# Kernel optimization log

Hardware: AMD Instinct MI355X
Metric: run time of the kernel (lower is better)

Reference implementation:

```python
import jax, jax.numpy as jnp
import numpy as np


def soft_threshold24(w):
    """2:4 soft-threshold along the last dim: in each contiguous group of 4,
    zero the two smallest magnitudes and shrink the two largest by the
    second-smallest magnitude (sign(w) * relu(|w| - t))."""
    M, N = w.shape
    g = w.reshape(M, N // 4, 4)
    a = jnp.abs(g)
    thr = jnp.sort(a, axis=-1)[..., 1:2]  # 2nd-smallest magnitude per group
    s = jnp.sign(g) * jnp.maximum(a - thr, 0.0)
    return s.reshape(M, N)


def mm_fp16(a, b):
    """fake_fp8_mm: cast operands to fp16, accumulate in fp32."""
    return jnp.matmul(a.astype(jnp.float16), b.astype(jnp.float16),
                      preferred_element_type=jnp.float32)


def setup_inputs() -> dict:
    key = jax.random.key(0)
    k0, k1, k2, k3 = jax.random.split(key, 4)
    B, S, D, R = 4, 2048, 2048, 512
    return {
        "x": jax.random.normal(k0, (B, S, D), jnp.float32),
        "weight_in": jax.random.normal(k1, (D, R), jnp.float32) * 0.02,
        "weight_out": jax.random.normal(k2, (D, R), jnp.float32) * 0.02,
        "bias": jax.random.normal(k3, (D,), jnp.float32) * 0.01,
        "sparse_scale_in": jnp.array(1.0, jnp.float32),
        "sparse_scale_out": jnp.array(1.0, jnp.float32),
    }


def reference(x, weight_in, weight_out, bias, sparse_scale_in, sparse_scale_out):
    B, S, D = x.shape
    # stage 1: x @ sparse24(weight_in) * scale_in  -> [B,S,R]
    win_s = soft_threshold24(weight_in) * sparse_scale_in          # [D, R]
    h = mm_fp16(x.reshape(-1, D), win_s)                            # [B*S, R] fp32
    # stage 2: h @ sparse24(weight_out.T) * scale_out + bias -> [B,S,D]
    wout_s = soft_threshold24(weight_out.T) * sparse_scale_out      # [R, D]
    out = mm_fp16(h, wout_s) + bias                                 # [B*S, D]
    return out.reshape(B, S, D)
```

## Files before the change

kernel.cpp:

```cpp
#include <hip/hip_runtime.h>

typedef _Float16 f16;
typedef _Float16 f16x8 __attribute__((ext_vector_type(8)));
typedef float f32x4 __attribute__((ext_vector_type(4)));

#define BK 32

__device__ __forceinline__ void g2l16(const f16* g, f16* l) {
    __builtin_amdgcn_global_load_lds(
        (const __attribute__((address_space(1))) void*)g,
        (__attribute__((address_space(3))) void*)l, 16, 0, 0);
}

__device__ __forceinline__ float soft1(float a, float thr, float w, float s) {
    return copysignf(fmaxf(a - thr, 0.0f), w) * s;
}

__device__ __forceinline__ float thr4(float a0, float a1, float a2, float a3) {
    float lo01 = fminf(a0, a1), hi01 = fmaxf(a0, a1);
    float lo23 = fminf(a2, a3), hi23 = fmaxf(a2, a3);
    return fminf(fmaxf(lo01, lo23), fminf(hi01, hi23));
}

__global__ __launch_bounds__(256) void prep_kernel(
    const float* __restrict__ x, f16* __restrict__ xh, int n8,
    const float* __restrict__ Wi, f16* __restrict__ winT, const float* __restrict__ sci,
    const float* __restrict__ Wo, f16* __restrict__ woutT, const float* __restrict__ sco,
    int D, int R, int nCastB, int nSpInB)
{
    int b = blockIdx.x;
    int tid = threadIdx.x;
    if (b < nCastB) {
        int i = b * 256 + tid;
        if (i < n8) {
            float4 a = reinterpret_cast<const float4*>(x)[2 * i];
            float4 c = reinterpret_cast<const float4*>(x)[2 * i + 1];
            f16x8 o = {(f16)a.x, (f16)a.y, (f16)a.z, (f16)a.w,
                       (f16)c.x, (f16)c.y, (f16)c.z, (f16)c.w};
            reinterpret_cast<f16x8*>(xh)[i] = o;
        }
    } else if (b < nCastB + nSpInB) {
        int t = (b - nCastB) * 256 + tid;
        int RG = R >> 2;
        if (t >= RG * D) return;
        int rg = t / D, d = t - rg * D;
        float s = *sci;
        float4 w = *reinterpret_cast<const float4*>(Wi + (size_t)d * R + rg * 4);
        float a0 = fabsf(w.x), a1 = fabsf(w.y), a2 = fabsf(w.z), a3 = fabsf(w.w);
        float thr = thr4(a0, a1, a2, a3);
        size_t base = (size_t)(rg * 4) * D + d;
        winT[base]                 = (f16)soft1(a0, thr, w.x, s);
        winT[base + D]             = (f16)soft1(a1, thr, w.y, s);
        winT[base + 2 * (size_t)D] = (f16)soft1(a2, thr, w.z, s);
        winT[base + 3 * (size_t)D] = (f16)soft1(a3, thr, w.w, s);
    } else {
        int t = (b - nCastB - nSpInB) * 256 + tid;
        if (t >= (D >> 2) * R) return;
        int dg = t / R, r = t - dg * R;
        float s = *sco;
        size_t i0 = (size_t)(dg * 4) * R + r;
        float w0 = Wo[i0], w1 = Wo[i0 + R], w2 = Wo[i0 + 2 * (size_t)R], w3 = Wo[i0 + 3 * (size_t)R];
        float a0 = fabsf(w0), a1 = fabsf(w1), a2 = fabsf(w2), a3 = fabsf(w3);
        float thr = thr4(a0, a1, a2, a3);
        woutT[i0]                 = (f16)soft1(a0, thr, w0, s);
        woutT[i0 + R]             = (f16)soft1(a1, thr, w1, s);
        woutT[i0 + 2 * (size_t)R] = (f16)soft1(a2, thr, w2, s);
        woutT[i0 + 3 * (size_t)R] = (f16)soft1(a3, thr, w3, s);
    }
}

template <int TBM, int TBN, typename OT, bool BIAS>
__global__ __launch_bounds__(256) void gemm_bt(
    const f16* __restrict__ A, const f16* __restrict__ Bt, OT* __restrict__ C,
    const float* __restrict__ bias, int M, int N, int K)
{
    constexpr int MI = TBM / 32;
    constexpr int NF = TBN / 32;
    constexpr int HM = TBM / 2;
    constexpr int HN = TBN / 2;
    __shared__ f16 As[2][TBM * BK];
    __shared__ f16 Bs[2][TBN * BK];

    const int tid  = threadIdx.x;
    const int lane = tid & 63;
    const int w    = tid >> 6;
    const int wm   = w & 1;
    const int wn   = w >> 1;
    const int l16  = lane & 15;
    const int quad = lane >> 4;

    const int nbx = N / TBN;
    const int nb  = gridDim.x;
    int d = blockIdx.x;
    int wgid = ((nb & 7) == 0) ? ((d & 7) * (nb >> 3) + (d >> 3)) : d;
    int by = wgid / nbx;
    int bx = wgid - by * nbx;
    const int bm = by * TBM;
    const int bn = bx * TBN;

    const int srow = lane >> 2;
    const int scol = (lane & 3) * 8;
    const f16* gA = A  + (size_t)(bm + w * (TBM / 4) + srow) * K + scol;
    const f16* gB = Bt + (size_t)(bn + w * (TBN / 4) + srow) * K + scol;

    f32x4 acc[MI][NF] = {};

    auto STAGE = [&](int buf, int k0) {
        f16* lA = &As[buf][(w * (TBM / 4)) * BK];
        f16* lB = &Bs[buf][(w * (TBN / 4)) * BK];
#pragma unroll
        for (int i = 0; i < TBM / 64; ++i)
            g2l16(gA + k0 + i * 16 * (size_t)K, lA + i * 16 * BK);
#pragma unroll
        for (int i = 0; i < TBN / 64; ++i)
            g2l16(gB + k0 + i * 16 * (size_t)K, lB + i * 16 * BK);
        __builtin_amdgcn_sched_barrier(0);
    };

    auto COMPUTE = [&](int buf) {
        f16x8 af[MI], bf[NF];
#pragma unroll
        for (int m = 0; m < MI; ++m)
            af[m] = *reinterpret_cast<const f16x8*>(
                &As[buf][(wm * HM + m * 16 + l16) * BK + quad * 8]);
#pragma unroll
        for (int n = 0; n < NF; ++n)
            bf[n] = *reinterpret_cast<const f16x8*>(
                &Bs[buf][(wn * HN + n * 16 + l16) * BK + quad * 8]);
#pragma unroll
        for (int m = 0; m < MI; ++m)
#pragma unroll
            for (int n = 0; n < NF; ++n)
                acc[m][n] = __builtin_amdgcn_mfma_f32_16x16x32_f16(af[m], bf[n], acc[m][n], 0, 0, 0);
    };

    const int nk = K / BK;
    STAGE(0, 0);
    __syncthreads();
    for (int t = 0; t < nk - 2; t += 2) {
        STAGE(1, (t + 1) * BK);
        COMPUTE(0);
        __syncthreads();
        STAGE(0, (t + 2) * BK);
        COMPUTE(1);
        __syncthreads();
    }
    STAGE(1, (nk - 1) * BK);
    COMPUTE(0);
    __syncthreads();
    COMPUTE(1);

#pragma unroll
    for (int m = 0; m < MI; ++m) {
        int row_base = bm + wm * HM + m * 16 + quad * 4;
#pragma unroll
        for (int n = 0; n < NF; ++n) {
            int col = bn + wn * HN + n * 16 + l16;
            float b = BIAS ? bias[col] : 0.0f;
#pragma unroll
            for (int r = 0; r < 4; ++r) {
                float v = acc[m][n][r];
                size_t idx = (size_t)(row_base + r) * N + col;
                if constexpr (BIAS) C[idx] = (OT)(v + b);
                else                C[idx] = (OT)v;
            }
        }
    }
}

extern "C" void kernel_launch(void* const* d_in, const int* in_sizes, int n_in,
                              void* d_out, int out_size, void* d_ws, size_t ws_size,
                              hipStream_t stream)
{
    const float* x      = (const float*)d_in[0];
    const float* w_in   = (const float*)d_in[1];
    const float* w_out  = (const float*)d_in[2];
    const float* bias   = (const float*)d_in[3];
    const float* sc_in  = (const float*)d_in[4];
    const float* sc_out = (const float*)d_in[5];

    const int D = in_sizes[3];
    const int R = in_sizes[1] / D;
    const int M = in_sizes[0] / D;

    f16* winT  = (f16*)d_ws;
    f16* woutT = winT + (size_t)R * D;
    f16* h     = woutT + (size_t)D * R;
    f16* xh    = h + (size_t)M * R;
    float* out = (float*)d_out;

    const int n8 = M * D / 8;
    const int nCastB  = (n8 + 255) / 256;
    const int nSpInB  = ((R / 4) * D + 255) / 256;
    const int nSpOutB = ((D / 4) * R + 255) / 256;
    prep_kernel<<<nCastB + nSpInB + nSpOutB, 256, 0, stream>>>(
        x, xh, n8, w_in, winT, sc_in, w_out, woutT, sc_out, D, R, nCastB, nSpInB);

    gemm_bt<64, 128, f16, false><<<(R / 128) * (M / 64), 256, 0, stream>>>(
        xh, winT, h, nullptr, M, R, D);
    gemm_bt<64, 128, float, true><<<(D / 128) * (M / 64), 256, 0, stream>>>(
        h, woutT, out, bias, M, D, R);
}
```

Measured before the change: 183.3 us.

## Restructure GEMM main loop with explicit vmcnt waits and fragment-before-prefetch ordering

```diff
diff --git a/kernel.cpp b/kernel.cpp
--- a/kernel.cpp
+++ b/kernel.cpp
@@ -11,6 +11,11 @@
         (const __attribute__((address_space(1))) void*)g,
         (__attribute__((address_space(3))) void*)l, 16, 0, 0);
 }
+
+template <int N> __device__ __forceinline__ void wait_vmcnt();
+template <> __device__ __forceinline__ void wait_vmcnt<0>() { asm volatile("s_waitcnt vmcnt(0)" ::: "memory"); }
+template <> __device__ __forceinline__ void wait_vmcnt<3>() { asm volatile("s_waitcnt vmcnt(3)" ::: "memory"); }
+template <> __device__ __forceinline__ void wait_vmcnt<4>() { asm volatile("s_waitcnt vmcnt(4)" ::: "memory"); }
 
 __device__ __forceinline__ float soft1(float a, float thr, float w, float s) {
     return copysignf(fmaxf(a - thr, 0.0f), w) * s;
@@ -78,6 +83,7 @@
     constexpr int NF = TBN / 32;
     constexpr int HM = TBM / 2;
     constexpr int HN = TBN / 2;
+    constexpr int L  = TBM / 64 + TBN / 64;
     __shared__ f16 As[2][TBM * BK];
     __shared__ f16 Bs[2][TBN * BK];
 
@@ -105,7 +111,8 @@
 
     f32x4 acc[MI][NF] = {};
 
-    auto STAGE = [&](int buf, int k0) {
+    auto STAGE = [&](int buf, int t) {
+        const int k0 = t * BK;
         f16* lA = &As[buf][(w * (TBM / 4)) * BK];
         f16* lB = &Bs[buf][(w * (TBN / 4)) * BK];
 #pragma unroll
@@ -114,11 +121,9 @@
 #pragma unroll
         for (int i = 0; i < TBN / 64; ++i)
             g2l16(gB + k0 + i * 16 * (size_t)K, lB + i * 16 * BK);
-        __builtin_amdgcn_sched_barrier(0);
     };
 
-    auto COMPUTE = [&](int buf) {
-        f16x8 af[MI], bf[NF];
+    auto LOADFRAG = [&](int buf, f16x8* af, f16x8* bf) {
 #pragma unroll
         for (int m = 0; m < MI; ++m)
             af[m] = *reinterpret_cast<const f16x8*>(
@@ -127,6 +132,9 @@
         for (int n = 0; n < NF; ++n)
             bf[n] = *reinterpret_cast<const f16x8*>(
                 &Bs[buf][(wn * HN + n * 16 + l16) * BK + quad * 8]);
+    };
+
+    auto MFMA_ALL = [&](f16x8* af, f16x8* bf) {
 #pragma unroll
         for (int m = 0; m < MI; ++m)
 #pragma unroll
@@ -136,19 +144,35 @@
 
     const int nk = K / BK;
     STAGE(0, 0);
-    __syncthreads();
-    for (int t = 0; t < nk - 2; t += 2) {
-        STAGE(1, (t + 1) * BK);
-        COMPUTE(0);
-        __syncthreads();
-        STAGE(0, (t + 2) * BK);
-        COMPUTE(1);
-        __syncthreads();
-    }
-    STAGE(1, (nk - 1) * BK);
-    COMPUTE(0);
-    __syncthreads();
-    COMPUTE(1);
+    STAGE(1, 1);
+    for (int t = 0; t < nk - 2; ++t) {
+        wait_vmcnt<L>();
+        __builtin_amdgcn_s_barrier();
+        __builtin_amdgcn_sched_barrier(0);
+        f16x8 af[MI], bf[NF];
+        LOADFRAG(t & 1, af, bf);
+        asm volatile("s_waitcnt lgkmcnt(0)" ::: "memory");
+        __builtin_amdgcn_sched_barrier(0);
+        __builtin_amdgcn_s_barrier();
+        STAGE(t & 1, t + 2);
+        MFMA_ALL(af, bf);
+    }
+    {
+        wait_vmcnt<L>();
+        __builtin_amdgcn_s_barrier();
+        __builtin_amdgcn_sched_barrier(0);
+        f16x8 af[MI], bf[NF];
+        LOADFRAG(nk & 1, af, bf);
+        MFMA_ALL(af, bf);
+    }
+    {
+        wait_vmcnt<0>();
+        __builtin_amdgcn_s_barrier();
+        __builtin_amdgcn_sched_barrier(0);
+        f16x8 af[MI], bf[NF];
+        LOADFRAG((nk - 1) & 1, af, bf);
+        MFMA_ALL(af, bf);
+    }
 
 #pragma unroll
     for (int m = 0; m < MI; ++m) {
@@ -198,6 +222,6 @@
 
     gemm_bt<64, 128, f16, false><<<(R / 128) * (M / 64), 256, 0, stream>>>(
         xh, winT, h, nullptr, M, R, D);
-    gemm_bt<64, 128, float, true><<<(D / 128) * (M / 64), 256, 0, stream>>>(
+    gemm_bt<128, 128, float, true><<<(D / 128) * (M / 128), 256, 0, stream>>>(
         h, woutT, out, bias, M, D, R);
 }
```

Measured after the change: 178.0 us. 1.03x faster.
